# Optimization experiments

Hardware: AMD Instinct MI355X
Metric: run time of the kernel (lower is better)

Reference implementation:

```python
import jax, jax.numpy as jnp
import numpy as np

H = 150  # hard-coded hidden size in the module

def _gru_cell(x, h, Wih, Whh, bih, bhh):
    # PyTorch GRUCell semantics: gates stacked [r, z, n]
    gi = x @ Wih.T + bih
    gh = h @ Whh.T + bhh
    ir, iz, in_ = jnp.split(gi, 3, axis=-1)
    hr, hz, hn = jnp.split(gh, 3, axis=-1)
    r = jax.nn.sigmoid(ir + hr)
    z = jax.nn.sigmoid(iz + hz)
    n = jnp.tanh(in_ + r * hn)
    return (1.0 - z) * n + z * h

def setup_inputs() -> dict:
    key = jax.random.key(0)
    ks = jax.random.split(key, 32)
    N, E, G = 100000, 500000, 16
    def lin(k, out_f, in_f):
        k1, k2 = jax.random.split(k)
        s = 1.0 / np.sqrt(in_f)
        W = jax.random.uniform(k1, (out_f, in_f), minval=-s, maxval=s, dtype=jnp.float32)
        b = jax.random.uniform(k2, (out_f,), minval=-s, maxval=s, dtype=jnp.float32)
        return W, b
    inp = {}
    inp['nodes'] = jax.random.normal(ks[0], (N, H), dtype=jnp.float32)
    inp['problem_type'] = jax.random.normal(ks[1], (G, 1), dtype=jnp.float32)
    inp['W1_0'], inp['b1_0'] = lin(ks[2], H, H)
    inp['W2_0'], inp['b2_0'] = lin(ks[3], H, H)
    inp['W1_1'], inp['b1_1'] = lin(ks[4], H, H)
    inp['W2_1'], inp['b2_1'] = lin(ks[5], H, H)
    inp['gru_Wih'], inp['gru_bih'] = lin(ks[6], 3 * H, H)
    inp['gru_Whh'], inp['gru_bhh'] = lin(ks[7], 3 * H, H)
    inp['fc1_W'], inp['fc1_b'] = lin(ks[8], 80, H + 1)
    inp['fc2_W'], inp['fc2_b'] = lin(ks[9], 80, 80)
    inp['fcL_W'], inp['fcL_b'] = lin(ks[10], 10, 80)
    inp['edges0'] = jax.random.randint(ks[11], (E, 2), 0, N, dtype=jnp.int32)
    inp['edges1'] = jax.random.randint(ks[12], (E, 2), 0, N, dtype=jnp.int32)
    inp['graph_ids'] = jnp.sort(jax.random.randint(ks[13], (N,), 0, G, dtype=jnp.int32))
    inp['passes'] = 4
    return inp

def reference(nodes, problem_type, W1_0, b1_0, W2_0, b2_0, W1_1, b1_1, W2_1, b2_1,
              gru_Wih, gru_bih, gru_Whh, gru_bhh, fc1_W, fc1_b, fc2_W, fc2_b,
              fcL_W, fcL_b, edges0, edges1, graph_ids, passes):
    G = problem_type.shape[0]
    edge_sets = [edges0, edges1]
    edge_params = [(W1_0, b1_0, W2_0, b2_0), (W1_1, b1_1, W2_1, b2_1)]
    h = nodes
    for j in range(passes):
        incoming = jnp.zeros_like(h)
        for e, (W1, b1, W2, b2) in zip(edge_sets, edge_params):
            src, dst = e[:, 1], e[:, 0]
            # gather -> Linear -> LeakyReLU -> Linear -> scatter-add
            y = jax.nn.leaky_relu(h[src] @ W1.T + b1)
            y = y @ W2.T + b2
            incoming = incoming.at[dst].add(y)
        h = _gru_cell(incoming, h, gru_Wih, gru_Whh, gru_bih, gru_bhh)
        if j < passes - 2:
            h = jax.lax.stop_gradient(h)  # mirrors .detach() in the original
    # per-graph sum pooling, then log with nan->0 and relu (so -inf -> 0 too)
    g = jax.ops.segment_sum(h, graph_ids, num_segments=G)
    lg = jnp.log(g)
    lg = jnp.where(jnp.isnan(lg), 0.0, lg)
    x = jax.nn.relu(lg)
    x = jnp.concatenate([x, problem_type], axis=1)  # [G, 151]
    x = jax.nn.leaky_relu(x @ fc1_W.T + fc1_b)
    x = jax.nn.leaky_relu(x @ fc2_W.T + fc2_b)
    return x @ fcL_W.T + fcL_b  # [G, 10]
```

## Files before the change

### kernel.cpp

```cpp
#include <hip/hip_runtime.h>

typedef unsigned short u16;
typedef unsigned int u32;
typedef __attribute__((ext_vector_type(8))) short s8v;
typedef __attribute__((ext_vector_type(8))) _Float16 h8v;
typedef __attribute__((ext_vector_type(4))) float f4v;

#define NN 100000
#define MROW 100096
#define EE 500000
#define GG 16
#define APIT 152
#define CPIT 160
#define CMAT (192*CPIT)
#define SCB 1024
#define SNB 98

__device__ __forceinline__ u16 f2h(float x){ union{u16 u;_Float16 f;}c; c.f=(_Float16)x; return c.u; }
__device__ __forceinline__ float h2f(u16 b){ union{u16 u;_Float16 f;}c; c.u=b; return (float)c.f; }

#define GLOAD_LDS(gp, lp) \
    __builtin_amdgcn_global_load_lds((const __attribute__((address_space(1))) void*)(gp), \
                                     (__attribute__((address_space(3))) void*)(lp), 16, 0, 0)

template<int NI>
__device__ __forceinline__ void stage(const u16* base, const int (&off)[NI], int koff,
                                      const int (&lds)[NI], u16* dst){
#pragma unroll
    for (int i=0;i<NI;i++) GLOAD_LDS(base+off[i]+koff, dst+lds[i]);
}

__device__ __forceinline__ void mf3h(const s8v (&af)[4], const u16* lWp, int wfo, int mstr,
                                     f4v (&X)[4], f4v (&Y)[4], f4v (&Z)[4]){
    h8v w0 = *(const h8v*)(lWp+wfo);
    h8v w1 = *(const h8v*)(lWp+mstr+wfo);
    h8v w2 = *(const h8v*)(lWp+2*mstr+wfo);
#pragma unroll
    for (int mi=0;mi<4;mi++){
        X[mi]=__builtin_amdgcn_mfma_f32_16x16x32_f16(*(const h8v*)&af[mi],w0,X[mi],0,0,0);
        Y[mi]=__builtin_amdgcn_mfma_f32_16x16x32_f16(*(const h8v*)&af[mi],w1,Y[mi],0,0,0);
        Z[mi]=__builtin_amdgcn_mfma_f32_16x16x32_f16(*(const h8v*)&af[mi],w2,Z[mi],0,0,0);
    }
}
__device__ __forceinline__ void mf2h(const s8v (&af)[4], const u16* lWp, int wfo, int mstr,
                                     f4v (&X)[4], f4v (&Y)[4]){
    h8v w0 = *(const h8v*)(lWp+wfo);
    h8v w1 = *(const h8v*)(lWp+mstr+wfo);
#pragma unroll
    for (int mi=0;mi<4;mi++){
        X[mi]=__builtin_amdgcn_mfma_f32_16x16x32_f16(*(const h8v*)&af[mi],w0,X[mi],0,0,0);
        Y[mi]=__builtin_amdgcn_mfma_f32_16x16x32_f16(*(const h8v*)&af[mi],w1,Y[mi],0,0,0);
    }
}

__device__ __forceinline__ void lda64(const u16* lA_, const int (&aF)[2][4], s8v (&a)[2][4]){
#pragma unroll
    for (int ks=0;ks<2;ks++)
#pragma unroll
        for (int mi=0;mi<4;mi++) a[ks][mi] = *(const s8v*)(lA_+aF[ks][mi]);
}
__device__ __forceinline__ void lda32(const u16* lA_, const int (&aF)[4], s8v (&a)[4]){
#pragma unroll
    for (int mi=0;mi<4;mi++) a[mi] = *(const s8v*)(lA_+aF[mi]);
}

__global__ __launch_bounds__(256,3) void k_ugemm2(const u16* __restrict__ H,
    const u16* __restrict__ W1h,
    const float* __restrict__ b1t0, const float* __restrict__ b1t1,
    u16* __restrict__ u0, u16* __restrict__ u1)
{
    __shared__ u16 lA[64*64], lW[2*64*64];
    int tid=threadIdx.x, wv=tid>>6, lane=tid&63, lr=lane&15, quad=lane>>4;
    int m0=blockIdx.x*64, n0=blockIdx.y*64;
    int aL64[2], aO64[2];
#pragma unroll
    for (int i=0;i<2;i++){ int s=tid+i*256, row=s>>3, q8=((s&7)^(row&7))<<3;
        aL64[i]=s<<3; aO64[i]=(m0+row)*APIT+q8; }
    int aL32[1], aO32[1];
    { int s=tid, row=s>>2, q8=((s&3)^(row&3))<<3; aL32[0]=s<<3; aO32[0]=(m0+row)*APIT+q8; }
    int wL64[4], wO64[4];
#pragma unroll
    for (int i=0;i<4;i++){ int s=tid+i*256, sel=s>>9, rem=s&511, row=rem>>3, q8=((rem&7)^(row&7))<<3;
        wL64[i]=sel*4096+rem*8; wO64[i]=sel*CMAT+(n0+row)*CPIT+q8; }
    int wL32[2], wO32[2];
#pragma unroll
    for (int i=0;i<2;i++){ int s=tid+i*256, sel=s>>8, rem=s&255, row=rem>>2, q8=((rem&3)^(row&3))<<3;
        wL32[i]=sel*2048+rem*8; wO32[i]=sel*CMAT+(n0+row)*CPIT+q8; }
    int aF64[2][4], wF64[2], aF32[4], wF32;
#pragma unroll
    for (int ks=0;ks<2;ks++){
#pragma unroll
        for (int mi=0;mi<4;mi++){ int row=mi*16+lr, ph=(ks*4+quad)^(row&7); aF64[ks][mi]=row*64+ph*8; }
        int wr=wv*16+lr, wp=(ks*4+quad)^(wr&7); wF64[ks]=wr*64+wp*8;
    }
#pragma unroll
    for (int mi=0;mi<4;mi++){ int row=mi*16+lr, ph=quad^(row&3); aF32[mi]=row*32+ph*8; }
    { int wr=wv*16+lr, wp=quad^(wr&3); wF32=wr*32+wp*8; }

    f4v a0[4]={}, a1[4]={};
    s8v a[2][4]; s8v a32[4];
#pragma unroll
    for (int kc=0;kc<2;kc++){
        int koff=kc*64;
        __syncthreads();
        stage<2>(H,aO64,koff,aL64,lA);
        stage<4>(W1h,wO64,koff,wL64,lW);
        __syncthreads();
        lda64(lA,aF64,a);
#pragma unroll
        for (int ks=0;ks<2;ks++) mf2h(a[ks],lW,wF64[ks],4096,a0,a1);
    }
    __syncthreads();
    stage<1>(H,aO32,128,aL32,lA);
    stage<2>(W1h,wO32,128,wL32,lW);
    __syncthreads();
    lda32(lA,aF32,a32);
    mf2h(a32,lW,wF32,2048,a0,a1);

    int c = n0 + wv*16 + lr;
    if (c < 152){
        float bb0=b1t0[c], bb1=b1t1[c];
#pragma unroll
        for (int mi=0;mi<4;mi++)
#pragma unroll
            for (int reg=0;reg<4;reg++){
                int r = m0 + mi*16 + quad*4 + reg;
                if (r >= NN) continue;
                float v0=a0[mi][reg]+bb0; v0 = v0>0.f ? v0 : 0.01f*v0;
                float v1=a1[mi][reg]+bb1; v1 = v1>0.f ? v1 : 0.01f*v1;
                if (c>=150){ v0=0.f; v1=0.f; }
                u0[(size_t)r*APIT+c]=f2h(v0);
                u1[(size_t)r*APIT+c]=f2h(v1);
            }
    }
}

__global__ __launch_bounds__(256,3) void k_mega(const u16* __restrict__ H,
    const u16* __restrict__ U0, const u16* __restrict__ U1,
    const u16* __restrict__ Cb,
    const u16* __restrict__ Wh,
    const float* __restrict__ tb, u16* __restrict__ Hn)
{
    __shared__ u16 lA[64*64], lW[3*64*64];
    int tid=threadIdx.x, wv=tid>>6, lane=tid&63, lr=lane&15, quad=lane>>4;
    int m0=blockIdx.x*64, n0=blockIdx.y*64;
    int aL64[2], aO64[2];
#pragma unroll
    for (int i=0;i<2;i++){ int s=tid+i*256, row=s>>3, q8=((s&7)^(row&7))<<3;
        aL64[i]=s<<3; aO64[i]=(m0+row)*APIT+q8; }
    int aL32[1], aO32[1];
    { int s=tid, row=s>>2, q8=((s&3)^(row&3))<<3; aL32[0]=s<<3; aO32[0]=(m0+row)*APIT+q8; }
    int wL64[6], wO64[6];
#pragma unroll
    for (int i=0;i<6;i++){ int s=tid+i*256, sel=s>>9, rem=s&511, row=rem>>3, q8=((rem&7)^(row&7))<<3;
        wL64[i]=sel*4096+rem*8; wO64[i]=sel*CMAT+(n0+row)*CPIT+q8; }
    int wL32[3], wO32[3];
#pragma unroll
    for (int i=0;i<3;i++){ int s=tid+i*256, sel=s>>8, rem=s&255, row=rem>>2, q8=((rem&3)^(row&3))<<3;
        wL32[i]=sel*2048+rem*8; wO32[i]=sel*CMAT+(n0+row)*CPIT+q8; }
    int aF64[2][4], wF64[2], aF32[4], wF32;
#pragma unroll
    for (int ks=0;ks<2;ks++){
#pragma unroll
        for (int mi=0;mi<4;mi++){ int row=mi*16+lr, ph=(ks*4+quad)^(row&7); aF64[ks][mi]=row*64+ph*8; }
        int wr=wv*16+lr, wp=(ks*4+quad)^(wr&7); wF64[ks]=wr*64+wp*8;
    }
#pragma unroll
    for (int mi=0;mi<4;mi++){ int row=mi*16+lr, ph=quad^(row&3); aF32[mi]=row*32+ph*8; }
    { int wr=wv*16+lr, wp=quad^(wr&3); wF32=wr*32+wp*8; }

    f4v aR[4]={}, aZ[4]={}, aI[4]={}, aHh[4]={};

    auto dopass = [&](const u16* A, const u16* Wg, f4v (&aT)[4]){
        s8v a[2][4]; s8v a32[4];
#pragma unroll
        for (int kc=0;kc<2;kc++){
            int koff=kc*64;
            __syncthreads();
            stage<2>(A,aO64,koff,aL64,lA);
            stage<6>(Wg,wO64,koff,wL64,lW);
            __syncthreads();
            lda64(lA,aF64,a);
#pragma unroll
            for (int ks=0;ks<2;ks++) mf3h(a[ks],lW,wF64[ks],4096,aR,aZ,aT);
        }
        __syncthreads();
        stage<1>(A,aO32,128,aL32,lA);
        stage<3>(Wg,wO32,128,wL32,lW);
        __syncthreads();
        lda32(lA,aF32,a32);
        mf3h(a32,lW,wF32,2048,aR,aZ,aT);
    };
    dopass(U0, Cb,          aI);
    dopass(U1, Cb + 3*CMAT, aI);
    dopass(H,  Wh,          aHh);

    int c = n0 + wv*16 + lr;
    if (c < 152){
        float bR=tb[c], bZ=tb[160+c], bI=tb[320+c], bHn=tb[480+c];
#pragma unroll
        for (int mi=0;mi<4;mi++)
#pragma unroll
            for (int reg=0;reg<4;reg++){
                int r = m0 + mi*16 + quad*4 + reg;
                if (r >= NN) continue;
                float pr=aR[mi][reg]+bR, pz=aZ[mi][reg]+bZ, pi=aI[mi][reg]+bI, ph_=aHh[mi][reg]+bHn;
                float rg = 1.f/(1.f+__expf(-pr));
                float zg = 1.f/(1.f+__expf(-pz));
                float e2 = __expf(2.f*(pi + rg*ph_));
                float n  = 1.f - 2.f/(e2+1.f);
                float hold = h2f(H[(size_t)r*APIT+c]);
                float o = (1.f-zg)*n + zg*hold;
                if (c>=150) o = 0.f;
                Hn[(size_t)r*APIT+c] = f2h(o);
            }
    }
}

__global__ void k_cast16(const float* __restrict__ src, int rowoff, u16* __restrict__ dst){
    int idx = blockIdx.x*256 + threadIdx.x;
    if (idx >= 192*160) return;
    int r = idx/160, c = idx - r*160;
    float x = (r<150 && c<150) ? src[(size_t)(rowoff+r)*150 + c] : 0.f;
    dst[(size_t)r*CPIT + c] = f2h(x);
}

__global__ void k_comp(const float* __restrict__ Wih, const float* __restrict__ W2_0,
                       const float* __restrict__ W2_1, const float* __restrict__ b2_0,
                       const float* __restrict__ b2_1, u16* __restrict__ Cb){
    int idx = blockIdx.x*256 + threadIdx.x;
    if (idx >= 6*192*160) return;
    int mat = idx/(192*160), rem = idx - mat*(192*160);
    int o = rem/160, c = rem - o*160;
    int s = mat/3, g = mat - s*3;
    float v = 0.f;
    if (o < 150){
        const float* wrow = Wih + (size_t)(g*150+o)*150;
        if (c < 150){
            const float* W2 = s ? W2_1 : W2_0;
            for (int j=0;j<150;j++) v += wrow[j] * W2[(size_t)j*150 + c];
        } else if (c==150 && s==0){
            for (int j=0;j<150;j++) v += wrow[j] * b2_0[j];
        } else if (c==151 && s==1){
            for (int j=0;j<150;j++) v += wrow[j] * b2_1[j];
        }
    }
    Cb[(size_t)mat*CMAT + o*CPIT + c] = f2h(v);
}

__global__ void k_tabs(const float* bih,const float* bhh,
                       const float* b1_0,const float* b1_1,
                       float* tb, float* b1t0, float* b1t1){
    int idx = blockIdx.x*256 + threadIdx.x;
    if (idx >= 6*160) return;
    int t = idx/160, c = idx - t*160;
    float v = 0.f;
    if (c < 150){
        if (t==0) v = bih[c]+bhh[c];
        else if (t==1) v = bih[150+c]+bhh[150+c];
        else if (t==2) v = bih[300+c];
        else if (t==3) v = bhh[300+c];
        else if (t==4) v = b1_0[c];
        else v = b1_1[c];
    }
    if (t<4) tb[t*160+c]=v;
    else if (t==4) b1t0[c]=v;
    else b1t1[c]=v;
}

__global__ void k_padfc1(const float* __restrict__ s, float* __restrict__ d){
    int idx = blockIdx.x*256 + threadIdx.x;
    if (idx >= 80*160) return;
    int r = idx/160, c = idx - r*160;
    d[idx] = (c<151) ? s[r*151 + c] : 0.f;
}

__global__ void k_inith(const float* __restrict__ nodes, u16* __restrict__ H){
    int idx = blockIdx.x*256 + threadIdx.x;
    if (idx >= NN*152) return;
    int m = idx/152, c = idx - m*152;
    float x = (c<150) ? nodes[(size_t)m*150 + c] : 0.f;
    H[(size_t)m*APIT + c] = f2h(x);
}

__global__ void k_hist2(const int* __restrict__ e0, const int* __restrict__ e1, int* __restrict__ hist){
    int e = blockIdx.x*256 + threadIdx.x;
    if (e >= EE) return;
    const int* ed = blockIdx.y ? e1 : e0;
    atomicAdd(&hist[blockIdx.y*NN + ed[2*e]], 1);
}

__global__ __launch_bounds__(256) void k_psum(const int* __restrict__ hist, int* __restrict__ part){
    int b = blockIdx.x, y = blockIdx.y, t = threadIdx.x;
    const int* cnt = hist + y*NN;
    int i0 = b*SCB + t*4;
    int s = 0;
#pragma unroll
    for (int u=0;u<4;u++){ int i=i0+u; if (i<NN) s += cnt[i]; }
#pragma unroll
    for (int o=32;o>0;o>>=1) s += __shfl_down(s,o);
    __shared__ int sd[4];
    if ((t&63)==0) sd[t>>6] = s;
    __syncthreads();
    if (t==0) part[y*128 + b] = sd[0]+sd[1]+sd[2]+sd[3];
}

__global__ __launch_bounds__(128) void k_pscan(int* __restrict__ part, int* __restrict__ off0, int* __restrict__ off1){
    int y = blockIdx.y, t = threadIdx.x;
    __shared__ int sd[128];
    int v = (t < SNB) ? part[y*128 + t] : 0;
    sd[t] = v;
    __syncthreads();
    for (int o=1;o<128;o<<=1){
        int x2 = 0;
        if (t >= o) x2 = sd[t-o];
        __syncthreads();
        if (t >= o) sd[t] += x2;
        __syncthreads();
    }
    if (t < SNB) part[y*128 + t] = sd[t] - v;
    if (t == 127){
        int* off = y ? off1 : off0;
        off[NN] = sd[127];
    }
}

__global__ __launch_bounds__(256) void k_papply(const int* __restrict__ hist, const int* __restrict__ part,
                                                int* __restrict__ off0, int* __restrict__ off1,
                                                int* __restrict__ cur){
    int b = blockIdx.x, y = blockIdx.y, t = threadIdx.x;
    const int* cnt = hist + y*NN;
    int* off = y ? off1 : off0;
    int* cu  = cur + y*NN;
    int i0 = b*SCB + t*4;
    int v[4]; int s = 0;
#pragma unroll
    for (int u=0;u<4;u++){ int i=i0+u; v[u] = (i<NN) ? cnt[i] : 0; s += v[u]; }
    __shared__ int sd[256];
    sd[t] = s;
    __syncthreads();
    for (int o=1;o<256;o<<=1){
        int x2 = 0;
        if (t >= o) x2 = sd[t-o];
        __syncthreads();
        if (t >= o) sd[t] += x2;
        __syncthreads();
    }
    int excl = part[y*128 + b] + sd[t] - s;
#pragma unroll
    for (int u=0;u<4;u++){
        int i = i0+u;
        if (i<NN){ off[i]=excl; cu[i]=excl; excl += v[u]; }
    }
}

__global__ void k_fill2(const int* __restrict__ e0, const int* __restrict__ e1,
                        int* __restrict__ cur, int* __restrict__ csr0, int* __restrict__ csr1){
    int e = blockIdx.x*256 + threadIdx.x;
    if (e >= EE) return;
    const int* ed = blockIdx.y ? e1 : e0;
    int* csr = blockIdx.y ? csr1 : csr0;
    int dst = ed[2*e], src = ed[2*e+1];
    int pos = atomicAdd(&cur[blockIdx.y*NN + dst], 1);
    csr[pos] = src;
}

__global__ void k_gath2(const u16* __restrict__ u0, const u16* __restrict__ u1,
                        const int* __restrict__ off0, const int* __restrict__ csr0,
                        const int* __restrict__ off1, const int* __restrict__ csr1,
                        u16* __restrict__ U0, u16* __restrict__ U1){
    int d = blockIdx.x*4 + (threadIdx.x>>6);
    if (d >= NN) return;
    int lane = threadIdx.x & 63;
    const u16* u = blockIdx.y ? u1 : u0;
    const int* off = blockIdx.y ? off1 : off0;
    const int* csr = blockIdx.y ? csr1 : csr0;
    u16* U = blockIdx.y ? U1 : U0;
    int e0 = off[d], e1 = off[d+1];
    bool tl = lane < 12;
    float s0=0.f, s1=0.f, t0=0.f, t1=0.f;
    int e = e0;
    for (; e+4 <= e1; e += 4){
        const u32* r0 = (const u32*)(u + (size_t)csr[e]  *APIT);
        const u32* r1 = (const u32*)(u + (size_t)csr[e+1]*APIT);
        const u32* r2 = (const u32*)(u + (size_t)csr[e+2]*APIT);
        const u32* r3 = (const u32*)(u + (size_t)csr[e+3]*APIT);
        u32 v0=r0[lane], v1=r1[lane], v2=r2[lane], v3=r3[lane];
        u32 w0=0, w1=0, w2=0, w3=0;
        if (tl){ w0=r0[64+lane]; w1=r1[64+lane]; w2=r2[64+lane]; w3=r3[64+lane]; }
        s0 += h2f((u16)(v0&0xffffu)) + h2f((u16)(v1&0xffffu)) + h2f((u16)(v2&0xffffu)) + h2f((u16)(v3&0xffffu));
        s1 += h2f((u16)(v0>>16))     + h2f((u16)(v1>>16))     + h2f((u16)(v2>>16))     + h2f((u16)(v3>>16));
        if (tl){
            t0 += h2f((u16)(w0&0xffffu)) + h2f((u16)(w1&0xffffu)) + h2f((u16)(w2&0xffffu)) + h2f((u16)(w3&0xffffu));
            t1 += h2f((u16)(w0>>16))     + h2f((u16)(w1>>16))     + h2f((u16)(w2>>16))     + h2f((u16)(w3>>16));
        }
    }
    for (; e < e1; e++){
        const u32* r = (const u32*)(u + (size_t)csr[e]*APIT);
        u32 v = r[lane];
        s0 += h2f((u16)(v & 0xffffu));
        s1 += h2f((u16)(v >> 16));
        if (tl){
            u32 w = r[64+lane];
            t0 += h2f((u16)(w & 0xffffu));
            t1 += h2f((u16)(w >> 16));
        }
    }
    if (lane == 11){ t0 = (float)(e1-e0); t1 = t0; }
    u32* Ur = (u32*)(U + (size_t)d*APIT);
    Ur[lane] = (u32)f2h(s0) | ((u32)f2h(s1) << 16);
    if (tl) Ur[64+lane] = (u32)f2h(t0) | ((u32)f2h(t1) << 16);
}

__global__ void k_seg(const u16* __restrict__ H, const int* __restrict__ gid, float* __restrict__ g){
    int f = threadIdx.x;
    if (f >= 150) return;
    int i0 = blockIdx.x*64;
    int i1 = i0 + 64; if (i1 > NN) i1 = NN;
    float acc = 0.f;
    int cg = gid[i0];
    for (int i=i0; i<i1; i++){
        int gg = gid[i];
        if (gg != cg){ atomicAdd(&g[cg*150+f], acc); acc=0.f; cg=gg; }
        acc += h2f(H[(size_t)i*APIT + f]);
    }
    atomicAdd(&g[cg*150+f], acc);
}

__global__ void k_mlp(const float* __restrict__ g, const float* __restrict__ pt,
                      const float* __restrict__ fc1p, const float* __restrict__ fc1b,
                      const float* __restrict__ fc2W, const float* __restrict__ fc2b,
                      const float* __restrict__ fcLW, const float* __restrict__ fcLb,
                      float* __restrict__ out){
    __shared__ float X[GG][152];
    __shared__ float Y[GG][80];
    __shared__ float Z[GG][80];
    int t = threadIdx.x;
    for (int idx=t; idx<GG*152; idx+=256){
        int gi=idx/152, c=idx-gi*152;
        float v = 0.f;
        if (c < 150){
            float lg = logf(g[gi*150+c]);
            if (lg != lg) lg = 0.f;
            v = fmaxf(lg, 0.f);
        } else if (c == 150) v = pt[gi];
        X[gi][c] = v;
    }
    __syncthreads();
    for (int idx=t; idx<GG*80; idx+=256){
        int gi=idx/80, o=idx-gi*80;
        float acc = fc1b[o];
        for (int k=0;k<151;k++) acc = fmaf(X[gi][k], fc1p[o*160+k], acc);
        Y[gi][o] = acc>0.f ? acc : 0.01f*acc;
    }
    __syncthreads();
    for (int idx=t; idx<GG*80; idx+=256){
        int gi=idx/80, o=idx-gi*80;
        float acc = fc2b[o];
        for (int k=0;k<80;k++) acc = fmaf(Y[gi][k], fc2W[o*80+k], acc);
        Z[gi][o] = acc>0.f ? acc : 0.01f*acc;
    }
    __syncthreads();
    for (int idx=t; idx<GG*10; idx+=256){
        int gi=idx/10, o=idx-gi*10;
        float acc = fcLb[o];
        for (int k=0;k<80;k++) acc = fmaf(Z[gi][k], fcLW[o*80+k], acc);
        out[idx] = acc;
    }
}

extern "C" void kernel_launch(void* const* d_in, const int* in_sizes, int n_in,
                              void* d_out, int out_size, void* d_ws, size_t ws_size,
                              hipStream_t stream) {
    const float* nodes = (const float*)d_in[0];
    const float* pt    = (const float*)d_in[1];
    const float* W1_0 = (const float*)d_in[2];  const float* b1_0 = (const float*)d_in[3];
    const float* W2_0 = (const float*)d_in[4];  const float* b2_0 = (const float*)d_in[5];
    const float* W1_1 = (const float*)d_in[6];  const float* b1_1 = (const float*)d_in[7];
    const float* W2_1 = (const float*)d_in[8];  const float* b2_1 = (const float*)d_in[9];
    const float* Wih = (const float*)d_in[10];  const float* bih = (const float*)d_in[11];
    const float* Whh = (const float*)d_in[12];  const float* bhh = (const float*)d_in[13];
    const float* fc1W = (const float*)d_in[14]; const float* fc1b = (const float*)d_in[15];
    const float* fc2W = (const float*)d_in[16]; const float* fc2b = (const float*)d_in[17];
    const float* fcLW = (const float*)d_in[18]; const float* fcLb = (const float*)d_in[19];
    const int* edges0 = (const int*)d_in[20];
    const int* edges1 = (const int*)d_in[21];
    const int* gid = (const int*)d_in[22];
    float* out = (float*)d_out;

    char* p = (char*)d_ws;
    auto alloc = [&](size_t bytes){ char* r = p; p += (bytes + 255) & ~(size_t)255; return r; };
    u16* XA  = (u16*)alloc((size_t)MROW*APIT*2);
    u16* XB  = (u16*)alloc((size_t)MROW*APIT*2);
    u16* U0  = (u16*)alloc((size_t)MROW*APIT*2);
    u16* U1  = (u16*)alloc((size_t)MROW*APIT*2);
    u16* Yu1 = (u16*)alloc((size_t)MROW*APIT*2);
    u16* W1h = (u16*)alloc((size_t)2*CMAT*2);
    u16* Wh  = (u16*)alloc((size_t)3*CMAT*2);
    u16* Cb  = (u16*)alloc((size_t)6*CMAT*2);
    float* tb   = (float*)alloc(4*160*4);
    float* b1t0 = (float*)alloc(160*4);
    float* b1t1 = (float*)alloc(160*4);
    float* fc1p = (float*)alloc(80*160*4);
    float* gbuf = (float*)alloc(GG*150*4);
    int* off0 = (int*)alloc((NN+1)*4);
    int* off1 = (int*)alloc((NN+1)*4);
    int* cur  = (int*)alloc((size_t)2*NN*4);
    int* hist = (int*)alloc((size_t)2*NN*4);
    int* part = (int*)alloc(2*128*4);
    int* csr0 = (int*)alloc((size_t)EE*4);
    int* csr1 = (int*)alloc((size_t)EE*4);
    (void)alloc(4096);

    k_cast16<<<120, 256, 0, stream>>>(W1_0, 0, W1h);
    k_cast16<<<120, 256, 0, stream>>>(W1_1, 0, W1h + CMAT);
    k_cast16<<<120, 256, 0, stream>>>(Whh, 0,   Wh);
    k_cast16<<<120, 256, 0, stream>>>(Whh, 150, Wh + CMAT);
    k_cast16<<<120, 256, 0, stream>>>(Whh, 300, Wh + 2*CMAT);
    k_comp<<<(6*192*160 + 255)/256, 256, 0, stream>>>(Wih, W2_0, W2_1, b2_0, b2_1, Cb);
    k_tabs<<<4, 256, 0, stream>>>(bih, bhh, b1_0, b1_1, tb, b1t0, b1t1);
    k_padfc1<<<50, 256, 0, stream>>>(fc1W, fc1p);
    k_inith<<<(NN*152 + 255)/256, 256, 0, stream>>>(nodes, XA);

    hipMemsetAsync(hist, 0, (size_t)2*NN*sizeof(int), stream);
    dim3 gE((EE+255)/256, 2), gS(SNB, 2), g1(1, 2);
    k_hist2<<<gE, 256, 0, stream>>>(edges0, edges1, hist);
    k_psum<<<gS, 256, 0, stream>>>(hist, part);
    k_pscan<<<g1, 128, 0, stream>>>(part, off0, off1);
    k_papply<<<gS, 256, 0, stream>>>(hist, part, off0, off1, cur);
    k_fill2<<<gE, 256, 0, stream>>>(edges0, edges1, cur, csr0, csr1);

    u16* Hc = XA; u16* Hx = XB;
    dim3 gT(MROW/64, 3);
    dim3 gGa((NN+3)/4, 2);
    for (int ps=0; ps<4; ps++){
        u16* yu0 = Hx;
        k_ugemm2<<<gT, 256, 0, stream>>>(Hc, W1h, b1t0, b1t1, yu0, Yu1);
        k_gath2<<<gGa, 256, 0, stream>>>(yu0, Yu1, off0, csr0, off1, csr1, U0, U1);
        k_mega<<<gT, 256, 0, stream>>>(Hc, U0, U1, Cb, Wh, tb, Hx);
        u16* t = Hc; Hc = Hx; Hx = t;
    }

    hipMemsetAsync(gbuf, 0, GG*150*sizeof(float), stream);
    k_seg<<<(NN+63)/64, 192, 0, stream>>>(Hc, gid, gbuf);
    k_mlp<<<1, 256, 0, stream>>>(gbuf, pt, fc1p, fc1b, fc2W, fc2b, fcLW, fcLb, out);
}
```

Baseline: 1.230 ms.

## Pre-swizzle weights into MFMA fragment layout and load them directly from global

```diff
diff --git a/kernel.cpp b/kernel.cpp
--- a/kernel.cpp
+++ b/kernel.cpp
@@ -11,8 +11,7 @@
 #define EE 500000
 #define GG 16
 #define APIT 152
-#define CPIT 160
-#define CMAT (192*CPIT)
+#define WFM 30720
 #define SCB 1024
 #define SNB 98
 
@@ -23,6 +22,10 @@
     __builtin_amdgcn_global_load_lds((const __attribute__((address_space(1))) void*)(gp), \
                                      (__attribute__((address_space(3))) void*)(lp), 16, 0, 0)
 
+__device__ __forceinline__ size_t widx(int row, int k){
+    return (size_t)(((row>>4)*5 + (k>>5))*512) + ((((k>>3)&3)*16 + (row&15))*8) + (k&7);
+}
+
 template<int NI>
 __device__ __forceinline__ void stage(const u16* base, const int (&off)[NI], int koff,
                                       const int (&lds)[NI], u16* dst){
@@ -30,11 +33,22 @@
     for (int i=0;i<NI;i++) GLOAD_LDS(base+off[i]+koff, dst+lds[i]);
 }
 
-__device__ __forceinline__ void mf3h(const s8v (&af)[4], const u16* lWp, int wfo, int mstr,
+__device__ __forceinline__ void lda64(const u16* lA_, const int (&aF)[2][4], s8v (&a)[2][4]){
+#pragma unroll
+    for (int ks=0;ks<2;ks++)
+#pragma unroll
+        for (int mi=0;mi<4;mi++) a[ks][mi] = *(const s8v*)(lA_+aF[ks][mi]);
+}
+__device__ __forceinline__ void lda32(const u16* lA_, const int (&aF)[4], s8v (&a)[4]){
+#pragma unroll
+    for (int mi=0;mi<4;mi++) a[mi] = *(const s8v*)(lA_+aF[mi]);
+}
+
+__device__ __forceinline__ void mf3d(const s8v (&af)[4], const u16* wp,
                                      f4v (&X)[4], f4v (&Y)[4], f4v (&Z)[4]){
-    h8v w0 = *(const h8v*)(lWp+wfo);
-    h8v w1 = *(const h8v*)(lWp+mstr+wfo);
-    h8v w2 = *(const h8v*)(lWp+2*mstr+wfo);
+    h8v w0 = *(const h8v*)(wp);
+    h8v w1 = *(const h8v*)(wp + WFM);
+    h8v w2 = *(const h8v*)(wp + 2*WFM);
 #pragma unroll
     for (int mi=0;mi<4;mi++){
         X[mi]=__builtin_amdgcn_mfma_f32_16x16x32_f16(*(const h8v*)&af[mi],w0,X[mi],0,0,0);
@@ -42,10 +56,10 @@
         Z[mi]=__builtin_amdgcn_mfma_f32_16x16x32_f16(*(const h8v*)&af[mi],w2,Z[mi],0,0,0);
     }
 }
-__device__ __forceinline__ void mf2h(const s8v (&af)[4], const u16* lWp, int wfo, int mstr,
+__device__ __forceinline__ void mf2d(const s8v (&af)[4], const u16* wp,
                                      f4v (&X)[4], f4v (&Y)[4]){
-    h8v w0 = *(const h8v*)(lWp+wfo);
-    h8v w1 = *(const h8v*)(lWp+mstr+wfo);
+    h8v w0 = *(const h8v*)(wp);
+    h8v w1 = *(const h8v*)(wp + WFM);
 #pragma unroll
     for (int mi=0;mi<4;mi++){
         X[mi]=__builtin_amdgcn_mfma_f32_16x16x32_f16(*(const h8v*)&af[mi],w0,X[mi],0,0,0);
@@ -53,23 +67,12 @@
     }
 }
 
-__device__ __forceinline__ void lda64(const u16* lA_, const int (&aF)[2][4], s8v (&a)[2][4]){
-#pragma unroll
-    for (int ks=0;ks<2;ks++)
-#pragma unroll
-        for (int mi=0;mi<4;mi++) a[ks][mi] = *(const s8v*)(lA_+aF[ks][mi]);
-}
-__device__ __forceinline__ void lda32(const u16* lA_, const int (&aF)[4], s8v (&a)[4]){
-#pragma unroll
-    for (int mi=0;mi<4;mi++) a[mi] = *(const s8v*)(lA_+aF[mi]);
-}
-
 __global__ __launch_bounds__(256,3) void k_ugemm2(const u16* __restrict__ H,
-    const u16* __restrict__ W1h,
+    const u16* __restrict__ W1f,
     const float* __restrict__ b1t0, const float* __restrict__ b1t1,
     u16* __restrict__ u0, u16* __restrict__ u1)
 {
-    __shared__ u16 lA[64*64], lW[2*64*64];
+    __shared__ u16 lA[64*64];
     int tid=threadIdx.x, wv=tid>>6, lane=tid&63, lr=lane&15, quad=lane>>4;
     int m0=blockIdx.x*64, n0=blockIdx.y*64;
     int aL64[2], aO64[2];
@@ -78,24 +81,15 @@
         aL64[i]=s<<3; aO64[i]=(m0+row)*APIT+q8; }
     int aL32[1], aO32[1];
     { int s=tid, row=s>>2, q8=((s&3)^(row&3))<<3; aL32[0]=s<<3; aO32[0]=(m0+row)*APIT+q8; }
-    int wL64[4], wO64[4];
-#pragma unroll
-    for (int i=0;i<4;i++){ int s=tid+i*256, sel=s>>9, rem=s&511, row=rem>>3, q8=((rem&7)^(row&7))<<3;
-        wL64[i]=sel*4096+rem*8; wO64[i]=sel*CMAT+(n0+row)*CPIT+q8; }
-    int wL32[2], wO32[2];
-#pragma unroll
-    for (int i=0;i<2;i++){ int s=tid+i*256, sel=s>>8, rem=s&255, row=rem>>2, q8=((rem&3)^(row&3))<<3;
-        wL32[i]=sel*2048+rem*8; wO32[i]=sel*CMAT+(n0+row)*CPIT+q8; }
-    int aF64[2][4], wF64[2], aF32[4], wF32;
-#pragma unroll
-    for (int ks=0;ks<2;ks++){
+    int aF64[2][4], aF32[4];
+#pragma unroll
+    for (int ks=0;ks<2;ks++)
 #pragma unroll
         for (int mi=0;mi<4;mi++){ int row=mi*16+lr, ph=(ks*4+quad)^(row&7); aF64[ks][mi]=row*64+ph*8; }
-        int wr=wv*16+lr, wp=(ks*4+quad)^(wr&7); wF64[ks]=wr*64+wp*8;
-    }
 #pragma unroll
     for (int mi=0;mi<4;mi++){ int row=mi*16+lr, ph=quad^(row&3); aF32[mi]=row*32+ph*8; }
-    { int wr=wv*16+lr, wp=quad^(wr&3); wF32=wr*32+wp*8; }
+    int jw = blockIdx.y*4 + wv;
+    const u16* Wp = W1f + (size_t)(jw*5)*512 + lane*8;
 
     f4v a0[4]={}, a1[4]={};
     s8v a[2][4]; s8v a32[4];
@@ -104,18 +98,16 @@
         int koff=kc*64;
         __syncthreads();
         stage<2>(H,aO64,koff,aL64,lA);
-        stage<4>(W1h,wO64,koff,wL64,lW);
         __syncthreads();
         lda64(lA,aF64,a);
 #pragma unroll
-        for (int ks=0;ks<2;ks++) mf2h(a[ks],lW,wF64[ks],4096,a0,a1);
+        for (int ks=0;ks<2;ks++) mf2d(a[ks], Wp + (kc*2+ks)*512, a0,a1);
     }
     __syncthreads();
     stage<1>(H,aO32,128,aL32,lA);
-    stage<2>(W1h,wO32,128,wL32,lW);
     __syncthreads();
     lda32(lA,aF32,a32);
-    mf2h(a32,lW,wF32,2048,a0,a1);
+    mf2d(a32, Wp + 4*512, a0,a1);
 
     int c = n0 + wv*16 + lr;
     if (c < 152){
@@ -137,11 +129,11 @@
 
 __global__ __launch_bounds__(256,3) void k_mega(const u16* __restrict__ H,
     const u16* __restrict__ U0, const u16* __restrict__ U1,
-    const u16* __restrict__ Cb,
-    const u16* __restrict__ Wh,
+    const u16* __restrict__ Cf,
+    const u16* __restrict__ Whf,
     const float* __restrict__ tb, u16* __restrict__ Hn)
 {
-    __shared__ u16 lA[64*64], lW[3*64*64];
+    __shared__ u16 lA[64*64];
     int tid=threadIdx.x, wv=tid>>6, lane=tid&63, lr=lane&15, quad=lane>>4;
     int m0=blockIdx.x*64, n0=blockIdx.y*64;
     int aL64[2], aO64[2];
@@ -150,50 +142,40 @@
         aL64[i]=s<<3; aO64[i]=(m0+row)*APIT+q8; }
     int aL32[1], aO32[1];
     { int s=tid, row=s>>2, q8=((s&3)^(row&3))<<3; aL32[0]=s<<3; aO32[0]=(m0+row)*APIT+q8; }
-    int wL64[6], wO64[6];
-#pragma unroll
-    for (int i=0;i<6;i++){ int s=tid+i*256, sel=s>>9, rem=s&511, row=rem>>3, q8=((rem&7)^(row&7))<<3;
-        wL64[i]=sel*4096+rem*8; wO64[i]=sel*CMAT+(n0+row)*CPIT+q8; }
-    int wL32[3], wO32[3];
-#pragma unroll
-    for (int i=0;i<3;i++){ int s=tid+i*256, sel=s>>8, rem=s&255, row=rem>>2, q8=((rem&3)^(row&3))<<3;
-        wL32[i]=sel*2048+rem*8; wO32[i]=sel*CMAT+(n0+row)*CPIT+q8; }
-    int aF64[2][4], wF64[2], aF32[4], wF32;
-#pragma unroll
-    for (int ks=0;ks<2;ks++){
+    int aF64[2][4], aF32[4];
+#pragma unroll
+    for (int ks=0;ks<2;ks++)
 #pragma unroll
         for (int mi=0;mi<4;mi++){ int row=mi*16+lr, ph=(ks*4+quad)^(row&7); aF64[ks][mi]=row*64+ph*8; }
-        int wr=wv*16+lr, wp=(ks*4+quad)^(wr&7); wF64[ks]=wr*64+wp*8;
-    }
 #pragma unroll
     for (int mi=0;mi<4;mi++){ int row=mi*16+lr, ph=quad^(row&3); aF32[mi]=row*32+ph*8; }
-    { int wr=wv*16+lr, wp=quad^(wr&3); wF32=wr*32+wp*8; }
+    int jw = blockIdx.y*4 + wv;
+    int laneoff = lane*8;
 
     f4v aR[4]={}, aZ[4]={}, aI[4]={}, aHh[4]={};
 
     auto dopass = [&](const u16* A, const u16* Wg, f4v (&aT)[4]){
+        const u16* Wp = Wg + (size_t)(jw*5)*512 + laneoff;
         s8v a[2][4]; s8v a32[4];
 #pragma unroll
         for (int kc=0;kc<2;kc++){
             int koff=kc*64;
             __syncthreads();
             stage<2>(A,aO64,koff,aL64,lA);
-            stage<6>(Wg,wO64,koff,wL64,lW);
             __syncthreads();
             lda64(lA,aF64,a);
 #pragma unroll
-            for (int ks=0;ks<2;ks++) mf3h(a[ks],lW,wF64[ks],4096,aR,aZ,aT);
+            for (int ks=0;ks<2;ks++) mf3d(a[ks], Wp + (kc*2+ks)*512, aR,aZ,aT);
         }
         __syncthreads();
         stage<1>(A,aO32,128,aL32,lA);
-        stage<3>(Wg,wO32,128,wL32,lW);
         __syncthreads();
         lda32(lA,aF32,a32);
-        mf3h(a32,lW,wF32,2048,aR,aZ,aT);
+        mf3d(a32, Wp + 4*512, aR,aZ,aT);
     };
-    dopass(U0, Cb,          aI);
-    dopass(U1, Cb + 3*CMAT, aI);
-    dopass(H,  Wh,          aHh);
+    dopass(U0, Cf,          aI);
+    dopass(U1, Cf + 3*WFM,  aI);
+    dopass(H,  Whf,         aHh);
 
     int c = n0 + wv*16 + lr;
     if (c < 152){
@@ -222,12 +204,12 @@
     if (idx >= 192*160) return;
     int r = idx/160, c = idx - r*160;
     float x = (r<150 && c<150) ? src[(size_t)(rowoff+r)*150 + c] : 0.f;
-    dst[(size_t)r*CPIT + c] = f2h(x);
+    dst[widx(r,c)] = f2h(x);
 }
 
 __global__ void k_comp(const float* __restrict__ Wih, const float* __restrict__ W2_0,
                        const float* __restrict__ W2_1, const float* __restrict__ b2_0,
-                       const float* __restrict__ b2_1, u16* __restrict__ Cb){
+                       const float* __restrict__ b2_1, u16* __restrict__ Cf){
     int idx = blockIdx.x*256 + threadIdx.x;
     if (idx >= 6*192*160) return;
     int mat = idx/(192*160), rem = idx - mat*(192*160);
@@ -245,7 +227,7 @@
             for (int j=0;j<150;j++) v += wrow[j] * b2_1[j];
         }
     }
-    Cb[(size_t)mat*CMAT + o*CPIT + c] = f2h(v);
+    Cf[(size_t)mat*WFM + widx(o,c)] = f2h(v);
 }
 
 __global__ void k_tabs(const float* bih,const float* bhh,
@@ -495,9 +477,9 @@
     u16* U0  = (u16*)alloc((size_t)MROW*APIT*2);
     u16* U1  = (u16*)alloc((size_t)MROW*APIT*2);
     u16* Yu1 = (u16*)alloc((size_t)MROW*APIT*2);
-    u16* W1h = (u16*)alloc((size_t)2*CMAT*2);
-    u16* Wh  = (u16*)alloc((size_t)3*CMAT*2);
-    u16* Cb  = (u16*)alloc((size_t)6*CMAT*2);
+    u16* W1f = (u16*)alloc((size_t)2*WFM*2);
+    u16* Whf = (u16*)alloc((size_t)3*WFM*2);
+    u16* Cf  = (u16*)alloc((size_t)6*WFM*2);
     float* tb   = (float*)alloc(4*160*4);
     float* b1t0 = (float*)alloc(160*4);
     float* b1t1 = (float*)alloc(160*4);
@@ -512,12 +494,12 @@
     int* csr1 = (int*)alloc((size_t)EE*4);
     (void)alloc(4096);
 
-    k_cast16<<<120, 256, 0, stream>>>(W1_0, 0, W1h);
-    k_cast16<<<120, 256, 0, stream>>>(W1_1, 0, W1h + CMAT);
-    k_cast16<<<120, 256, 0, stream>>>(Whh, 0,   Wh);
-    k_cast16<<<120, 256, 0, stream>>>(Whh, 150, Wh + CMAT);
-    k_cast16<<<120, 256, 0, stream>>>(Whh, 300, Wh + 2*CMAT);
-    k_comp<<<(6*192*160 + 255)/256, 256, 0, stream>>>(Wih, W2_0, W2_1, b2_0, b2_1, Cb);
+    k_cast16<<<120, 256, 0, stream>>>(W1_0, 0, W1f);
+    k_cast16<<<120, 256, 0, stream>>>(W1_1, 0, W1f + WFM);
+    k_cast16<<<120, 256, 0, stream>>>(Whh, 0,   Whf);
+    k_cast16<<<120, 256, 0, stream>>>(Whh, 150, Whf + WFM);
+    k_cast16<<<120, 256, 0, stream>>>(Whh, 300, Whf + 2*WFM);
+    k_comp<<<(6*192*160 + 255)/256, 256, 0, stream>>>(Wih, W2_0, W2_1, b2_0, b2_1, Cf);
     k_tabs<<<4, 256, 0, stream>>>(bih, bhh, b1_0, b1_1, tb, b1t0, b1t1);
     k_padfc1<<<50, 256, 0, stream>>>(fc1W, fc1p);
     k_inith<<<(NN*152 + 255)/256, 256, 0, stream>>>(nodes, XA);
@@ -535,9 +517,9 @@
     dim3 gGa((NN+3)/4, 2);
     for (int ps=0; ps<4; ps++){
         u16* yu0 = Hx;
-        k_ugemm2<<<gT, 256, 0, stream>>>(Hc, W1h, b1t0, b1t1, yu0, Yu1);
+        k_ugemm2<<<gT, 256, 0, stream>>>(Hc, W1f, b1t0, b1t1, yu0, Yu1);
         k_gath2<<<gGa, 256, 0, stream>>>(yu0, Yu1, off0, csr0, off1, csr1, U0, U1);
-        k_mega<<<gT, 256, 0, stream>>>(Hc, U0, U1, Cb, Wh, tb, Hx);
+        k_mega<<<gT, 256, 0, stream>>>(Hc, U0, U1, Cf, Whf, tb, Hx);
         u16* t = Hc; Hc = Hx; Hx = t;
     }
 
```

After: 1.198 ms. -2.6%, faster.
